# Optimization experiments

Measured on AMD Instinct MI355X. Metric: run time of the kernel, lower is better.

The kernel has to match this reference:

```python
import jax, jax.numpy as jnp
import numpy as np

B, H, L, D = 1, 8, 2048, 64
DP = 3   # positional coord dim
RE = 1   # extra relative features appended via concat
F = DP + RE  # LazyLinear in-features


def setup_inputs() -> dict:
    key = jax.random.key(0)
    ks = jax.random.split(key, 12)
    return {
        "q": jax.random.normal(ks[0], (B, H, L, D), jnp.float32),
        "k": jax.random.normal(ks[1], (B, H, L, D), jnp.float32),
        "v": jax.random.normal(ks[2], (B, H, L, D), jnp.float32),
        "c": jax.random.uniform(ks[3], (B, 1, 1, L), jnp.float32),
        "d_q": jax.random.normal(ks[4], (B, L, DP), jnp.float32),
        "d_k_top": jax.random.normal(ks[5], (B, L, DP), jnp.float32),
        "d_k_bot": jax.random.normal(ks[6], (B, L, DP), jnp.float32),
        "d_k_score": jax.random.uniform(ks[7], (B, L, 2, F), jnp.float32),
        "relative_top": jax.random.normal(ks[8], (B, L, L, RE), jnp.float32),
        "relative_bottom": jax.random.normal(ks[9], (B, L, L, RE), jnp.float32),
        "W_w": jax.random.normal(ks[10], (F, H), jnp.float32) * 0.1,
        "W_b": jax.random.normal(ks[11], (F, H), jnp.float32) * 0.1,
    }


def _pairwise_diff(a, b):
    # a: [B,Lq,Dp], b: [B,Lk,Dp] -> [B,Lq,Lk,Dp]
    return a[:, :, None, :] - b[:, None, :, :]


def reference(q, k, v, c, d_q, d_k_top, d_k_bot, d_k_score,
              relative_top, relative_bottom, W_w, W_b):
    # score function: scaled dot product -> [B,H,Lq,Lk]
    scores = jnp.einsum('bhqd,bhkd->bhqk', q, k) * (q.shape[-1] ** -0.5)

    # relative-position bias path
    dt = jnp.concatenate([_pairwise_diff(d_q, d_k_top), relative_top], axis=-1)     # [B,Lq,Lk,F]
    db = jnp.concatenate([_pairwise_diff(d_q, d_k_bot), relative_bottom], axis=-1)  # [B,Lq,Lk,F]
    dm = jnp.stack([dt, db], axis=3)                 # [B,Lq,Lk,2,F]
    dm = dm * d_k_score[:, None]                     # broadcast over Lq
    dm = dm.sum(axis=3)                              # [B,Lq,Lk,F]

    w = jax.nn.softplus(dm @ W_w).transpose(0, 3, 1, 2)  # [B,H,Lq,Lk]
    b = (dm @ W_b).transpose(0, 3, 1, 2)                 # [B,H,Lq,Lk]
    scores = scores * w + b

    # leaky probability function: softmax gated by per-key sampling weights c
    probs = jax.nn.softmax(scores, axis=-1) * c      # [B,H,Lq,Lk]

    out = jnp.einsum('bhqk,bhkd->bhqd', probs, v)
    return out, probs
```

## Files before the change

### kernel.cpp

```cpp
#include <hip/hip_runtime.h>
#include <cstdint>
#include <cstddef>

#define NH 8
#define LQ 2048
#define DH 64
#define NKT_HALF 16

typedef __attribute__((ext_vector_type(8))) __bf16 bf16x8;
typedef __attribute__((ext_vector_type(8))) unsigned short ushort8;
typedef __attribute__((ext_vector_type(4))) float floatx4;

__device__ __forceinline__ unsigned short bf_trunc(float x) {
    return (unsigned short)(__float_as_uint(x) >> 16);
}
__device__ __forceinline__ float bf_up(unsigned short h) {
    return __uint_as_float(((unsigned int)h) << 16);
}
__device__ __forceinline__ unsigned short bf_rne(float x) {
    unsigned int u = __float_as_uint(x);
    return (unsigned short)((u + 0x7FFFu + ((u >> 16) & 1u)) >> 16);
}
struct hl_t { unsigned short h, l; };
__device__ __forceinline__ hl_t split2(float x) {
    hl_t r;
    r.h = bf_trunc(x);
    r.l = bf_trunc(x - bf_up(r.h));
    return r;
}

#define MFMA16(A, B, C) __builtin_amdgcn_mfma_f32_16x16x32_bf16((A), (B), (C), 0, 0, 0)

__global__ __launch_bounds__(256) void prep_kernel(
    const float* __restrict__ kp,  const float* __restrict__ vp,
    const float* __restrict__ cp,  const float* __restrict__ dktp,
    const float* __restrict__ dkbp,const float* __restrict__ dksp,
    const float* __restrict__ Wwp, const float* __restrict__ Wbp,
    unsigned short* __restrict__ khig, unsigned short* __restrict__ klog,
    unsigned short* __restrict__ vhig, unsigned short* __restrict__ vlog,
    float* __restrict__ metag)
{
    const int bid = blockIdx.x;
    const int t   = threadIdx.x;

    if (bid < 256) {
        const int h = bid >> 5, kt = bid & 31;
        const int row = t >> 2, s = t & 3;
        const size_t kg = (size_t)(h * LQ) + kt * 64 + row;
        const float* src = kp + kg * DH + s * 16;
        unsigned short* dh_ = khig + kg * DH + s * 16;
        unsigned short* dl_ = klog + kg * DH + s * 16;
        ushort8 vh0, vh1, vl0, vl1;
#pragma unroll
        for (int j = 0; j < 2; ++j) {
            float4 x = *(const float4*)(src + 4 * j);
            hl_t a = split2(x.x * 0.125f), b = split2(x.y * 0.125f);
            hl_t c = split2(x.z * 0.125f), d = split2(x.w * 0.125f);
            vh0[4*j+0]=a.h; vl0[4*j+0]=a.l; vh0[4*j+1]=b.h; vl0[4*j+1]=b.l;
            vh0[4*j+2]=c.h; vl0[4*j+2]=c.l; vh0[4*j+3]=d.h; vl0[4*j+3]=d.l;
        }
#pragma unroll
        for (int j = 0; j < 2; ++j) {
            float4 x = *(const float4*)(src + 8 + 4 * j);
            hl_t a = split2(x.x * 0.125f), b = split2(x.y * 0.125f);
            hl_t c = split2(x.z * 0.125f), d = split2(x.w * 0.125f);
            vh1[4*j+0]=a.h; vl1[4*j+0]=a.l; vh1[4*j+1]=b.h; vl1[4*j+1]=b.l;
            vh1[4*j+2]=c.h; vl1[4*j+2]=c.l; vh1[4*j+3]=d.h; vl1[4*j+3]=d.l;
        }
        *(ushort8*)&dh_[0] = vh0; *(ushort8*)&dh_[8] = vh1;
        *(ushort8*)&dl_[0] = vl0; *(ushort8*)&dl_[8] = vl1;
    } else if (bid < 512) {
        const int h = (bid - 256) >> 5, kt = (bid - 256) & 31;
        const int p = t >> 4, mm = t & 15;
        const int k0 = kt * 64;
#pragma unroll
        for (int g = 0; g < 2; ++g) {
            const int kka = 2 * p + 32 * g;
            const float ca = cp[k0 + kka], cb = cp[k0 + kka + 1];
            const float* va = vp + ((size_t)(h * LQ + k0 + kka)) * DH;
            const float* vb = va + DH;
#pragma unroll
            for (int dd = 0; dd < 4; ++dd) {
                const int d = mm + 16 * dd;
                hl_t xa = split2(va[d] * ca);
                hl_t xb = split2(vb[d] * cb);
                const size_t base = ((size_t)(h * 32 + kt) * 64 + d) * 64 + kka;
                *(unsigned int*)&vhig[base] = (unsigned int)xa.h | ((unsigned int)xb.h << 16);
                *(unsigned int*)&vlog[base] = (unsigned int)xa.l | ((unsigned int)xb.l << 16);
            }
        }
    } else {
        const int idx = (bid - 512) * 256 + t;
        const int h  = idx >> 11;
        const int kg = idx & 2047;
        float Ww[4], Wb[4];
#pragma unroll
        for (int f = 0; f < 4; ++f) { Ww[f] = Wwp[f * NH + h]; Wb[f] = Wbp[f * NH + h]; }
        const float* sc_ = dksp + (size_t)kg * 8;
        const float* tp  = dktp + (size_t)kg * 3;
        const float* bt  = dkbp + (size_t)kg * 3;
        float* mo = metag + ((size_t)(h * LQ) + kg) * 12;
        float cw = 0.f, cb2 = 0.f;
#pragma unroll
        for (int f = 0; f < 3; ++f) {
            const float stf = sc_[f], sbf = sc_[4 + f];
            const float A  = stf + sbf;
            const float Bv = tp[f] * stf + bt[f] * sbf;
            mo[f]     = A * Ww[f];
            mo[4 + f] = A * Wb[f];
            cw  -= Bv * Ww[f];
            cb2 -= Bv * Wb[f];
        }
        mo[3]  = cw;              mo[7]  = cb2;
        mo[8]  = sc_[3] * Ww[3];  mo[9]  = sc_[7] * Ww[3];
        mo[10] = sc_[3] * Wb[3];  mo[11] = sc_[7] * Wb[3];
    }
}

template<int PRE>
__global__ __launch_bounds__(256, 3) void attn_main(
    const float* __restrict__ qp,  const float* __restrict__ kp,
    const float* __restrict__ vp,  const float* __restrict__ cp,
    const float* __restrict__ dqp, const float* __restrict__ dktp,
    const float* __restrict__ dkbp,const float* __restrict__ dksp,
    const float* __restrict__ rtp, const float* __restrict__ rbp,
    const float* __restrict__ Wwp, const float* __restrict__ Wbp,
    const unsigned short* __restrict__ khig, const unsigned short* __restrict__ klog,
    const unsigned short* __restrict__ vhig, const unsigned short* __restrict__ vlog,
    const float* __restrict__ metag,
    float* __restrict__ probp, float* __restrict__ lws, float* __restrict__ pvws)
{
    __shared__ unsigned short sh_khi[64 * 72];
    __shared__ unsigned short sh_klo[64 * 72];
    __shared__ unsigned short sh_vhi[64 * 72];
    __shared__ unsigned short sh_vlo[64 * 72];
    __shared__ float sh_meta[64 * 12];
    __shared__ float sh_dqs[64 * 3];

    const int bid  = blockIdx.x;
    const int half = bid & 1;
    const int h    = (bid >> 1) & 7;
    const int qt   = bid >> 4;
    const int q0   = qt * 64;
    const int t    = threadIdx.x;
    const int lane = t & 63;
    const int m    = lane & 15;
    const int quad = lane >> 4;
    const int w16  = (t >> 6) * 16;

    float Ww[4], Wb[4];
    if constexpr (!PRE) {
#pragma unroll
        for (int f = 0; f < 4; ++f) { Ww[f] = Wwp[f * NH + h]; Wb[f] = Wbp[f * NH + h]; }
    }

    {
        const int row = t >> 2, s = t & 3;
        const float* src = qp + ((size_t)(h * LQ + q0 + row)) * DH + s * 16;
        ushort8 vh0, vh1, vl0, vl1;
#pragma unroll
        for (int j = 0; j < 2; ++j) {
            float4 x = *(const float4*)(src + 4 * j);
            hl_t a = split2(x.x), b = split2(x.y), c = split2(x.z), d = split2(x.w);
            vh0[4*j+0]=a.h; vl0[4*j+0]=a.l; vh0[4*j+1]=b.h; vl0[4*j+1]=b.l;
            vh0[4*j+2]=c.h; vl0[4*j+2]=c.l; vh0[4*j+3]=d.h; vl0[4*j+3]=d.l;
        }
#pragma unroll
        for (int j = 0; j < 2; ++j) {
            float4 x = *(const float4*)(src + 8 + 4 * j);
            hl_t a = split2(x.x), b = split2(x.y), c = split2(x.z), d = split2(x.w);
            vh1[4*j+0]=a.h; vl1[4*j+0]=a.l; vh1[4*j+1]=b.h; vl1[4*j+1]=b.l;
            vh1[4*j+2]=c.h; vl1[4*j+2]=c.l; vh1[4*j+3]=d.h; vl1[4*j+3]=d.l;
        }
        const int base = row * 72 + s * 16;
        *(ushort8*)&sh_khi[base] = vh0;  *(ushort8*)&sh_khi[base + 8] = vh1;
        *(ushort8*)&sh_klo[base] = vl0;  *(ushort8*)&sh_klo[base + 8] = vl1;
        if (t < 64) {
            sh_dqs[t * 3 + 0] = dqp[(q0 + t) * 3 + 0];
            sh_dqs[t * 3 + 1] = dqp[(q0 + t) * 3 + 1];
            sh_dqs[t * 3 + 2] = dqp[(q0 + t) * 3 + 2];
        }
    }
    __syncthreads();

    bf16x8 aqh[2], aql[2];
#pragma unroll
    for (int kc = 0; kc < 2; ++kc) {
        aqh[kc] = *(const bf16x8*)&sh_khi[(w16 + m) * 72 + kc * 32 + quad * 8];
        aql[kc] = *(const bf16x8*)&sh_klo[(w16 + m) * 72 + kc * 32 + quad * 8];
    }
    float dq0[4], dq1[4], dq2[4];
#pragma unroll
    for (int r = 0; r < 4; ++r) {
        const int row = w16 + quad * 4 + r;
        dq0[r] = sh_dqs[row * 3 + 0]; dq1[r] = sh_dqs[row * 3 + 1]; dq2[r] = sh_dqs[row * 3 + 2];
    }
    __syncthreads();

    const floatx4 zf = {0.f, 0.f, 0.f, 0.f};
    floatx4 pacc[4] = {zf, zf, zf, zf};
    float lpart[4] = {0.f, 0.f, 0.f, 0.f};

    for (int kth = 0; kth < NKT_HALF; ++kth) {
        const int k0 = (half * NKT_HALF + kth) * 64;

        if constexpr (PRE) {
            {
                const int row = t >> 2, s = t & 3;
                const size_t gb = ((size_t)(h * LQ) + k0 + row) * DH + s * 16;
                const int base = row * 72 + s * 16;
                *(ushort8*)&sh_khi[base]     = *(const ushort8*)&khig[gb];
                *(ushort8*)&sh_khi[base + 8] = *(const ushort8*)&khig[gb + 8];
                *(ushort8*)&sh_klo[base]     = *(const ushort8*)&klog[gb];
                *(ushort8*)&sh_klo[base + 8] = *(const ushort8*)&klog[gb + 8];
            }
            {
                const int row = t >> 2, s = t & 3;
                const size_t gb = ((size_t)(h * 32 + (k0 >> 6)) * 64 + row) * 64 + s * 16;
                const int base = row * 72 + s * 16;
                *(ushort8*)&sh_vhi[base]     = *(const ushort8*)&vhig[gb];
                *(ushort8*)&sh_vhi[base + 8] = *(const ushort8*)&vhig[gb + 8];
                *(ushort8*)&sh_vlo[base]     = *(const ushort8*)&vlog[gb];
                *(ushort8*)&sh_vlo[base + 8] = *(const ushort8*)&vlog[gb + 8];
            }
            if (t < 192) {
                const int k = t / 3, j = t - k * 3;
                const float4 mv = *(const float4*)(metag + ((size_t)(h * LQ) + k0 + k) * 12 + j * 4);
                *(float4*)&sh_meta[k * 12 + j * 4] = mv;
            }
        } else {
            {
                const int row = t >> 2, s = t & 3;
                const float* src = kp + ((size_t)(h * LQ + k0 + row)) * DH + s * 16;
                ushort8 vh0, vh1, vl0, vl1;
#pragma unroll
                for (int j = 0; j < 2; ++j) {
                    float4 x = *(const float4*)(src + 4 * j);
                    hl_t a = split2(x.x), b = split2(x.y), c = split2(x.z), d = split2(x.w);
                    vh0[4*j+0]=a.h; vl0[4*j+0]=a.l; vh0[4*j+1]=b.h; vl0[4*j+1]=b.l;
                    vh0[4*j+2]=c.h; vl0[4*j+2]=c.l; vh0[4*j+3]=d.h; vl0[4*j+3]=d.l;
                }
#pragma unroll
                for (int j = 0; j < 2; ++j) {
                    float4 x = *(const float4*)(src + 8 + 4 * j);
                    hl_t a = split2(x.x), b = split2(x.y), c = split2(x.z), d = split2(x.w);
                    vh1[4*j+0]=a.h; vl1[4*j+0]=a.l; vh1[4*j+1]=b.h; vl1[4*j+1]=b.l;
                    vh1[4*j+2]=c.h; vl1[4*j+2]=c.l; vh1[4*j+3]=d.h; vl1[4*j+3]=d.l;
                }
                const int base = row * 72 + s * 16;
                *(ushort8*)&sh_khi[base] = vh0;  *(ushort8*)&sh_khi[base + 8] = vh1;
                *(ushort8*)&sh_klo[base] = vl0;  *(ushort8*)&sh_klo[base + 8] = vl1;
            }
            {
                const int p = t >> 4;
                const int mm = t & 15;
#pragma unroll
                for (int g = 0; g < 2; ++g) {
                    const int kka = 2 * p + 32 * g;
                    const float ca = cp[k0 + kka], cb = cp[k0 + kka + 1];
                    const float* va = vp + ((size_t)(h * LQ + k0 + kka)) * DH;
                    const float* vb = va + DH;
#pragma unroll
                    for (int dd = 0; dd < 4; ++dd) {
                        const int d = mm + 16 * dd;
                        hl_t xa = split2(va[d] * ca);
                        hl_t xb = split2(vb[d] * cb);
                        *(unsigned int*)&sh_vhi[d * 72 + kka] = (unsigned int)xa.h | ((unsigned int)xb.h << 16);
                        *(unsigned int*)&sh_vlo[d * 72 + kka] = (unsigned int)xa.l | ((unsigned int)xb.l << 16);
                    }
                }
            }
            if (t < 64) {
                const int kg = k0 + t;
                const float* sc_ = dksp + (size_t)kg * 8;
                const float* tp  = dktp + (size_t)kg * 3;
                const float* bt  = dkbp + (size_t)kg * 3;
                float cw = 0.f, cb2 = 0.f;
#pragma unroll
                for (int f = 0; f < 3; ++f) {
                    const float stf = sc_[f], sbf = sc_[4 + f];
                    const float A  = stf + sbf;
                    const float Bv = tp[f] * stf + bt[f] * sbf;
                    sh_meta[t * 12 + f]     = A * Ww[f];
                    sh_meta[t * 12 + 4 + f] = A * Wb[f];
                    cw  -= Bv * Ww[f];
                    cb2 -= Bv * Wb[f];
                }
                sh_meta[t * 12 + 3]  = cw;              sh_meta[t * 12 + 7]  = cb2;
                sh_meta[t * 12 + 8]  = sc_[3] * Ww[3];  sh_meta[t * 12 + 9]  = sc_[7] * Ww[3];
                sh_meta[t * 12 + 10] = sc_[3] * Wb[3];  sh_meta[t * 12 + 11] = sc_[7] * Wb[3];
            }
        }
        __syncthreads();

        float rt_[4][4], rb_[4][4];
#pragma unroll
        for (int r = 0; r < 4; ++r) {
            const size_t q = (size_t)(q0 + w16 + quad * 4 + r);
#pragma unroll
            for (int nt = 0; nt < 4; ++nt) {
                rt_[nt][r] = rtp[q * LQ + k0 + nt * 16 + m];
                rb_[nt][r] = rbp[q * LQ + k0 + nt * 16 + m];
            }
        }

        floatx4 sc[4] = {zf, zf, zf, zf};
#pragma unroll
        for (int nt = 0; nt < 4; ++nt) {
#pragma unroll
            for (int kc = 0; kc < 2; ++kc) {
                const int kb = (nt * 16 + m) * 72 + kc * 32 + quad * 8;
                bf16x8 bh = *(const bf16x8*)&sh_khi[kb];
                bf16x8 bl = *(const bf16x8*)&sh_klo[kb];
                sc[nt] = MFMA16(aqh[kc], bh, sc[nt]);
                sc[nt] = MFMA16(aql[kc], bh, sc[nt]);
                sc[nt] = MFMA16(aqh[kc], bl, sc[nt]);
            }
        }
        __syncthreads();

        unsigned short* ebf = sh_klo;
#pragma unroll
        for (int nt = 0; nt < 4; ++nt) {
            const int kcol = nt * 16 + m;
            const float m0 = sh_meta[kcol * 12 + 0],  m1 = sh_meta[kcol * 12 + 1];
            const float m2 = sh_meta[kcol * 12 + 2],  m3 = sh_meta[kcol * 12 + 3];
            const float m4 = sh_meta[kcol * 12 + 4],  m5 = sh_meta[kcol * 12 + 5];
            const float m6 = sh_meta[kcol * 12 + 6],  m7 = sh_meta[kcol * 12 + 7];
            const float m8 = sh_meta[kcol * 12 + 8],  m9 = sh_meta[kcol * 12 + 9];
            const float mA = sh_meta[kcol * 12 + 10], mB = sh_meta[kcol * 12 + 11];
#pragma unroll
            for (int r = 0; r < 4; ++r) {
                float ww = fmaf(dq0[r], m0, m3); ww = fmaf(dq1[r], m1, ww); ww = fmaf(dq2[r], m2, ww);
                ww = fmaf(rt_[nt][r], m8, ww);   ww = fmaf(rb_[nt][r], m9, ww);
                float bb = fmaf(dq0[r], m4, m7); bb = fmaf(dq1[r], m5, bb); bb = fmaf(dq2[r], m6, bb);
                bb = fmaf(rt_[nt][r], mA, bb);   bb = fmaf(rb_[nt][r], mB, bb);
                const float wg = fmaxf(ww, 0.f) + __logf(1.f + __expf(-fabsf(ww)));
                float sv;
                if constexpr (PRE) sv = fmaf(sc[nt][r], wg, bb);
                else               sv = fmaf(sc[nt][r] * 0.125f, wg, bb);
                const float e  = __expf(sv - 8.0f);
                lpart[r] += e;
                probp[((size_t)(h * LQ + q0 + w16 + quad * 4 + r)) * LQ + k0 + kcol] = e;
                ebf[(w16 + quad * 4 + r) * 72 + kcol] = bf_rne(e);
            }
        }

        bf16x8 ap0 = *(const bf16x8*)&ebf[(w16 + m) * 72 + quad * 8];
        bf16x8 ap1 = *(const bf16x8*)&ebf[(w16 + m) * 72 + 32 + quad * 8];
#pragma unroll
        for (int nt = 0; nt < 4; ++nt) {
            const int vb = (nt * 16 + m) * 72 + quad * 8;
            bf16x8 bh0 = *(const bf16x8*)&sh_vhi[vb];
            bf16x8 bl0 = *(const bf16x8*)&sh_vlo[vb];
            bf16x8 bh1 = *(const bf16x8*)&sh_vhi[vb + 32];
            bf16x8 bl1 = *(const bf16x8*)&sh_vlo[vb + 32];
            pacc[nt] = MFMA16(ap0, bh0, pacc[nt]);
            pacc[nt] = MFMA16(ap0, bl0, pacc[nt]);
            pacc[nt] = MFMA16(ap1, bh1, pacc[nt]);
            pacc[nt] = MFMA16(ap1, bl1, pacc[nt]);
        }
        __syncthreads();
    }

#pragma unroll
    for (int off = 1; off < 16; off <<= 1) {
#pragma unroll
        for (int r = 0; r < 4; ++r) lpart[r] += __shfl_xor(lpart[r], off, 64);
    }
    if (m == 0) {
#pragma unroll
        for (int r = 0; r < 4; ++r)
            lws[half * (NH * LQ) + h * LQ + q0 + w16 + quad * 4 + r] = lpart[r];
    }
#pragma unroll
    for (int nt = 0; nt < 4; ++nt) {
#pragma unroll
        for (int r = 0; r < 4; ++r) {
            const size_t row = (size_t)(h * LQ + q0 + w16 + quad * 4 + r);
            pvws[(size_t)half * (NH * LQ * DH) + row * DH + nt * 16 + m] = pacc[nt][r];
        }
    }
}

__global__ void combine_kernel(const float* __restrict__ pvws, const float* __restrict__ lws,
                               float* __restrict__ outp)
{
    const int idx4 = blockIdx.x * 256 + threadIdx.x;
    const int row  = idx4 >> 4;
    const int d4   = (idx4 & 15) * 4;
    const float4 a = *(const float4*)(pvws + (size_t)row * DH + d4);
    const float4 b = *(const float4*)(pvws + (size_t)(NH * LQ * DH) + (size_t)row * DH + d4);
    const float rl = 1.0f / (lws[row] + lws[NH * LQ + row]);
    *(float4*)(outp + (size_t)row * DH + d4) =
        make_float4((a.x + b.x) * rl, (a.y + b.y) * rl, (a.z + b.z) * rl, (a.w + b.w) * rl);
}

__global__ void norm_kernel(float* __restrict__ probp, const float* __restrict__ cp,
                            const float* __restrict__ lws)
{
    const int row = blockIdx.x;
    const float rl = 1.0f / (lws[row] + lws[NH * LQ + row]);
    float* p = probp + (size_t)row * LQ;
    const int t = threadIdx.x;
    float4 x0 = *(const float4*)(p + t * 4);
    float4 x1 = *(const float4*)(p + (t + 256) * 4);
    const float4 c0 = *(const float4*)(cp + t * 4);
    const float4 c1 = *(const float4*)(cp + (t + 256) * 4);
    x0.x *= rl * c0.x; x0.y *= rl * c0.y; x0.z *= rl * c0.z; x0.w *= rl * c0.w;
    x1.x *= rl * c1.x; x1.y *= rl * c1.y; x1.z *= rl * c1.z; x1.w *= rl * c1.w;
    *(float4*)(p + t * 4)         = x0;
    *(float4*)(p + (t + 256) * 4) = x1;
}

extern "C" void kernel_launch(void* const* d_in, const int* in_sizes, int n_in,
                              void* d_out, int out_size, void* d_ws, size_t ws_size,
                              hipStream_t stream)
{
    (void)in_sizes; (void)n_in; (void)out_size;
    const float* qp   = (const float*)d_in[0];
    const float* kp   = (const float*)d_in[1];
    const float* vp   = (const float*)d_in[2];
    const float* cp   = (const float*)d_in[3];
    const float* dqp  = (const float*)d_in[4];
    const float* dktp = (const float*)d_in[5];
    const float* dkbp = (const float*)d_in[6];
    const float* dksp = (const float*)d_in[7];
    const float* rtp  = (const float*)d_in[8];
    const float* rbp  = (const float*)d_in[9];
    const float* Wwp  = (const float*)d_in[10];
    const float* Wbp  = (const float*)d_in[11];

    float* outp  = (float*)d_out;
    float* probp = (float*)d_out + (size_t)NH * LQ * DH;

    float* lws  = (float*)d_ws;
    float* pvws = lws + 2 * (NH * LQ);
    unsigned short* khig = (unsigned short*)(pvws + (size_t)2 * NH * LQ * DH);
    unsigned short* klog = khig + (size_t)NH * LQ * DH;
    unsigned short* vhig = klog + (size_t)NH * LQ * DH;
    unsigned short* vlog = vhig + (size_t)NH * LQ * DH;
    float* metag = (float*)(vlog + (size_t)NH * LQ * DH);

    const size_t need = (size_t)2 * NH * LQ * 4
                      + (size_t)2 * NH * LQ * DH * 4
                      + (size_t)4 * NH * LQ * DH * 2
                      + (size_t)NH * LQ * 12 * 4;

    if (ws_size >= need) {
        prep_kernel<<<dim3(576), dim3(256), 0, stream>>>(
            kp, vp, cp, dktp, dkbp, dksp, Wwp, Wbp, khig, klog, vhig, vlog, metag);
        attn_main<1><<<dim3(512), dim3(256), 0, stream>>>(
            qp, kp, vp, cp, dqp, dktp, dkbp, dksp, rtp, rbp, Wwp, Wbp,
            khig, klog, vhig, vlog, metag, probp, lws, pvws);
    } else {
        attn_main<0><<<dim3(512), dim3(256), 0, stream>>>(
            qp, kp, vp, cp, dqp, dktp, dkbp, dksp, rtp, rbp, Wwp, Wbp,
            nullptr, nullptr, nullptr, nullptr, nullptr, probp, lws, pvws);
    }
    combine_kernel<<<dim3(1024), dim3(256), 0, stream>>>(pvws, lws, outp);
    norm_kernel<<<dim3(NH * LQ), dim3(256), 0, stream>>>(probp, cp, lws);
}
```

Measured before the change: 287.3 us.

## Prefetch next K/V/meta tile into registers and fuse norm with combine

Removes the non-precomputed fallback path, so the precomputed split-bf16 K/V tiles are always used. The main loop now loads the next tile's K/V/meta into registers while the current tile is being computed, which hides global load latency behind the math. Launch bounds drop from 3 to 2 waves per SIMD to make room for the extra registers. The separate combine and norm kernels become one kernel that handles 8 rows per block, cutting a launch and reusing the c vector across rows. The trade-off is lower occupancy, and the workspace size check is dropped.

Result: no change. 286.2 us (-0.4%).

```diff
diff --git a/kernel.cpp b/kernel.cpp
--- a/kernel.cpp
+++ b/kernel.cpp
@@ -117,14 +117,9 @@
     }
 }
 
-template<int PRE>
-__global__ __launch_bounds__(256, 3) void attn_main(
-    const float* __restrict__ qp,  const float* __restrict__ kp,
-    const float* __restrict__ vp,  const float* __restrict__ cp,
-    const float* __restrict__ dqp, const float* __restrict__ dktp,
-    const float* __restrict__ dkbp,const float* __restrict__ dksp,
+__global__ __launch_bounds__(256, 2) void attn_main(
+    const float* __restrict__ qp,  const float* __restrict__ dqp,
     const float* __restrict__ rtp, const float* __restrict__ rbp,
-    const float* __restrict__ Wwp, const float* __restrict__ Wbp,
     const unsigned short* __restrict__ khig, const unsigned short* __restrict__ klog,
     const unsigned short* __restrict__ vhig, const unsigned short* __restrict__ vlog,
     const float* __restrict__ metag,
@@ -148,15 +143,27 @@
     const int quad = lane >> 4;
     const int w16  = (t >> 6) * 16;
 
-    float Ww[4], Wb[4];
-    if constexpr (!PRE) {
-#pragma unroll
-        for (int f = 0; f < 4; ++f) { Ww[f] = Wwp[f * NH + h]; Wb[f] = Wbp[f * NH + h]; }
-    }
+    const int srow = t >> 2, ss = t & 3;
+    const int sbase = srow * 72 + ss * 16;
+    const int mk = t / 3, mj = t - mk * 3;
+
+    size_t kgb = ((size_t)(h * LQ) + half * NKT_HALF * 64 + srow) * DH + ss * 16;
+    size_t vgb = ((size_t)(h * 32 + half * NKT_HALF) * 64 + srow) * 64 + ss * 16;
+    size_t mgb = ((size_t)(h * LQ) + half * NKT_HALF * 64 + mk) * 12 + mj * 4;
+
+    ushort8 rkh0 = *(const ushort8*)&khig[kgb];
+    ushort8 rkh1 = *(const ushort8*)&khig[kgb + 8];
+    ushort8 rkl0 = *(const ushort8*)&klog[kgb];
+    ushort8 rkl1 = *(const ushort8*)&klog[kgb + 8];
+    ushort8 rvh0 = *(const ushort8*)&vhig[vgb];
+    ushort8 rvh1 = *(const ushort8*)&vhig[vgb + 8];
+    ushort8 rvl0 = *(const ushort8*)&vlog[vgb];
+    ushort8 rvl1 = *(const ushort8*)&vlog[vgb + 8];
+    float4  rmeta;
+    if (t < 192) rmeta = *(const float4*)&metag[mgb];
 
     {
-        const int row = t >> 2, s = t & 3;
-        const float* src = qp + ((size_t)(h * LQ + q0 + row)) * DH + s * 16;
+        const float* src = qp + ((size_t)(h * LQ + q0 + srow)) * DH + ss * 16;
         ushort8 vh0, vh1, vl0, vl1;
 #pragma unroll
         for (int j = 0; j < 2; ++j) {
@@ -172,9 +179,8 @@
             vh1[4*j+0]=a.h; vl1[4*j+0]=a.l; vh1[4*j+1]=b.h; vl1[4*j+1]=b.l;
             vh1[4*j+2]=c.h; vl1[4*j+2]=c.l; vh1[4*j+3]=d.h; vl1[4*j+3]=d.l;
         }
-        const int base = row * 72 + s * 16;
-        *(ushort8*)&sh_khi[base] = vh0;  *(ushort8*)&sh_khi[base + 8] = vh1;
-        *(ushort8*)&sh_klo[base] = vl0;  *(ushort8*)&sh_klo[base + 8] = vl1;
+        *(ushort8*)&sh_khi[sbase] = vh0;  *(ushort8*)&sh_khi[sbase + 8] = vh1;
+        *(ushort8*)&sh_klo[sbase] = vl0;  *(ushort8*)&sh_klo[sbase + 8] = vl1;
         if (t < 64) {
             sh_dqs[t * 3 + 0] = dqp[(q0 + t) * 3 + 0];
             sh_dqs[t * 3 + 1] = dqp[(q0 + t) * 3 + 1];
@@ -204,94 +210,31 @@
     for (int kth = 0; kth < NKT_HALF; ++kth) {
         const int k0 = (half * NKT_HALF + kth) * 64;
 
-        if constexpr (PRE) {
-            {
-                const int row = t >> 2, s = t & 3;
-                const size_t gb = ((size_t)(h * LQ) + k0 + row) * DH + s * 16;
-                const int base = row * 72 + s * 16;
-                *(ushort8*)&sh_khi[base]     = *(const ushort8*)&khig[gb];
-                *(ushort8*)&sh_khi[base + 8] = *(const ushort8*)&khig[gb + 8];
-                *(ushort8*)&sh_klo[base]     = *(const ushort8*)&klog[gb];
-                *(ushort8*)&sh_klo[base + 8] = *(const ushort8*)&klog[gb + 8];
-            }
-            {
-                const int row = t >> 2, s = t & 3;
-                const size_t gb = ((size_t)(h * 32 + (k0 >> 6)) * 64 + row) * 64 + s * 16;
-                const int base = row * 72 + s * 16;
-                *(ushort8*)&sh_vhi[base]     = *(const ushort8*)&vhig[gb];
-                *(ushort8*)&sh_vhi[base + 8] = *(const ushort8*)&vhig[gb + 8];
-                *(ushort8*)&sh_vlo[base]     = *(const ushort8*)&vlog[gb];
-                *(ushort8*)&sh_vlo[base + 8] = *(const ushort8*)&vlog[gb + 8];
-            }
-            if (t < 192) {
-                const int k = t / 3, j = t - k * 3;
-                const float4 mv = *(const float4*)(metag + ((size_t)(h * LQ) + k0 + k) * 12 + j * 4);
-                *(float4*)&sh_meta[k * 12 + j * 4] = mv;
-            }
-        } else {
-            {
-                const int row = t >> 2, s = t & 3;
-                const float* src = kp + ((size_t)(h * LQ + k0 + row)) * DH + s * 16;
-                ushort8 vh0, vh1, vl0, vl1;
-#pragma unroll
-                for (int j = 0; j < 2; ++j) {
-                    float4 x = *(const float4*)(src + 4 * j);
-                    hl_t a = split2(x.x), b = split2(x.y), c = split2(x.z), d = split2(x.w);
-                    vh0[4*j+0]=a.h; vl0[4*j+0]=a.l; vh0[4*j+1]=b.h; vl0[4*j+1]=b.l;
-                    vh0[4*j+2]=c.h; vl0[4*j+2]=c.l; vh0[4*j+3]=d.h; vl0[4*j+3]=d.l;
-                }
-#pragma unroll
-                for (int j = 0; j < 2; ++j) {
-                    float4 x = *(const float4*)(src + 8 + 4 * j);
-                    hl_t a = split2(x.x), b = split2(x.y), c = split2(x.z), d = split2(x.w);
-                    vh1[4*j+0]=a.h; vl1[4*j+0]=a.l; vh1[4*j+1]=b.h; vl1[4*j+1]=b.l;
-                    vh1[4*j+2]=c.h; vl1[4*j+2]=c.l; vh1[4*j+3]=d.h; vl1[4*j+3]=d.l;
-                }
-                const int base = row * 72 + s * 16;
-                *(ushort8*)&sh_khi[base] = vh0;  *(ushort8*)&sh_khi[base + 8] = vh1;
-                *(ushort8*)&sh_klo[base] = vl0;  *(ushort8*)&sh_klo[base + 8] = vl1;
-            }
-            {
-                const int p = t >> 4;
-                const int mm = t & 15;
-#pragma unroll
-                for (int g = 0; g < 2; ++g) {
-                    const int kka = 2 * p + 32 * g;
-                    const float ca = cp[k0 + kka], cb = cp[k0 + kka + 1];
-                    const float* va = vp + ((size_t)(h * LQ + k0 + kka)) * DH;
-                    const float* vb = va + DH;
-#pragma unroll
-                    for (int dd = 0; dd < 4; ++dd) {
-                        const int d = mm + 16 * dd;
-                        hl_t xa = split2(va[d] * ca);
-                        hl_t xb = split2(vb[d] * cb);
-                        *(unsigned int*)&sh_vhi[d * 72 + kka] = (unsigned int)xa.h | ((unsigned int)xb.h << 16);
-                        *(unsigned int*)&sh_vlo[d * 72 + kka] = (unsigned int)xa.l | ((unsigned int)xb.l << 16);
-                    }
-                }
-            }
-            if (t < 64) {
-                const int kg = k0 + t;
-                const float* sc_ = dksp + (size_t)kg * 8;
-                const float* tp  = dktp + (size_t)kg * 3;
-                const float* bt  = dkbp + (size_t)kg * 3;
-                float cw = 0.f, cb2 = 0.f;
-#pragma unroll
-                for (int f = 0; f < 3; ++f) {
-                    const float stf = sc_[f], sbf = sc_[4 + f];
-                    const float A  = stf + sbf;
-                    const float Bv = tp[f] * stf + bt[f] * sbf;
-                    sh_meta[t * 12 + f]     = A * Ww[f];
-                    sh_meta[t * 12 + 4 + f] = A * Wb[f];
-                    cw  -= Bv * Ww[f];
-                    cb2 -= Bv * Wb[f];
-                }
-                sh_meta[t * 12 + 3]  = cw;              sh_meta[t * 12 + 7]  = cb2;
-                sh_meta[t * 12 + 8]  = sc_[3] * Ww[3];  sh_meta[t * 12 + 9]  = sc_[7] * Ww[3];
-                sh_meta[t * 12 + 10] = sc_[3] * Wb[3];  sh_meta[t * 12 + 11] = sc_[7] * Wb[3];
-            }
-        }
+        *(ushort8*)&sh_khi[sbase]     = rkh0;
+        *(ushort8*)&sh_khi[sbase + 8] = rkh1;
+        *(ushort8*)&sh_klo[sbase]     = rkl0;
+        *(ushort8*)&sh_klo[sbase + 8] = rkl1;
+        *(ushort8*)&sh_vhi[sbase]     = rvh0;
+        *(ushort8*)&sh_vhi[sbase + 8] = rvh1;
+        *(ushort8*)&sh_vlo[sbase]     = rvl0;
+        *(ushort8*)&sh_vlo[sbase + 8] = rvl1;
+        if (t < 192) *(float4*)&sh_meta[mk * 12 + mj * 4] = rmeta;
         __syncthreads();
+
+        if (kth + 1 < NKT_HALF) {
+            kgb += (size_t)64 * DH;
+            vgb += (size_t)64 * 64;
+            mgb += (size_t)64 * 12;
+            rkh0 = *(const ushort8*)&khig[kgb];
+            rkh1 = *(const ushort8*)&khig[kgb + 8];
+            rkl0 = *(const ushort8*)&klog[kgb];
+            rkl1 = *(const ushort8*)&klog[kgb + 8];
+            rvh0 = *(const ushort8*)&vhig[vgb];
+            rvh1 = *(const ushort8*)&vhig[vgb + 8];
+            rvl0 = *(const ushort8*)&vlog[vgb];
+            rvl1 = *(const ushort8*)&vlog[vgb + 8];
+            if (t < 192) rmeta = *(const float4*)&metag[mgb];
+        }
 
         float rt_[4][4], rb_[4][4];
 #pragma unroll
@@ -336,9 +279,7 @@
                 float bb = fmaf(dq0[r], m4, m7); bb = fmaf(dq1[r], m5, bb); bb = fmaf(dq2[r], m6, bb);
                 bb = fmaf(rt_[nt][r], mA, bb);   bb = fmaf(rb_[nt][r], mB, bb);
                 const float wg = fmaxf(ww, 0.f) + __logf(1.f + __expf(-fabsf(ww)));
-                float sv;
-                if constexpr (PRE) sv = fmaf(sc[nt][r], wg, bb);
-                else               sv = fmaf(sc[nt][r] * 0.125f, wg, bb);
+                const float sv = fmaf(sc[nt][r], wg, bb);
                 const float e  = __expf(sv - 8.0f);
                 lpart[r] += e;
                 probp[((size_t)(h * LQ + q0 + w16 + quad * 4 + r)) * LQ + k0 + kcol] = e;
@@ -383,41 +324,43 @@
     }
 }
 
-__global__ void combine_kernel(const float* __restrict__ pvws, const float* __restrict__ lws,
-                               float* __restrict__ outp)
+__global__ __launch_bounds__(256) void norm_combine(
+    float* __restrict__ probp, const float* __restrict__ cp,
+    const float* __restrict__ lws, const float* __restrict__ pvws,
+    float* __restrict__ outp)
 {
-    const int idx4 = blockIdx.x * 256 + threadIdx.x;
-    const int row  = idx4 >> 4;
-    const int d4   = (idx4 & 15) * 4;
-    const float4 a = *(const float4*)(pvws + (size_t)row * DH + d4);
-    const float4 b = *(const float4*)(pvws + (size_t)(NH * LQ * DH) + (size_t)row * DH + d4);
-    const float rl = 1.0f / (lws[row] + lws[NH * LQ + row]);
-    *(float4*)(outp + (size_t)row * DH + d4) =
-        make_float4((a.x + b.x) * rl, (a.y + b.y) * rl, (a.z + b.z) * rl, (a.w + b.w) * rl);
-}
-
-__global__ void norm_kernel(float* __restrict__ probp, const float* __restrict__ cp,
-                            const float* __restrict__ lws)
-{
-    const int row = blockIdx.x;
-    const float rl = 1.0f / (lws[row] + lws[NH * LQ + row]);
-    float* p = probp + (size_t)row * LQ;
-    const int t = threadIdx.x;
-    float4 x0 = *(const float4*)(p + t * 4);
-    float4 x1 = *(const float4*)(p + (t + 256) * 4);
+    __shared__ float rl8[8];
+    const int t    = threadIdx.x;
+    const int row0 = blockIdx.x * 8;
     const float4 c0 = *(const float4*)(cp + t * 4);
     const float4 c1 = *(const float4*)(cp + (t + 256) * 4);
-    x0.x *= rl * c0.x; x0.y *= rl * c0.y; x0.z *= rl * c0.z; x0.w *= rl * c0.w;
-    x1.x *= rl * c1.x; x1.y *= rl * c1.y; x1.z *= rl * c1.z; x1.w *= rl * c1.w;
-    *(float4*)(p + t * 4)         = x0;
-    *(float4*)(p + (t + 256) * 4) = x1;
+    if (t < 8) rl8[t] = 1.0f / (lws[row0 + t] + lws[NH * LQ + row0 + t]);
+    __syncthreads();
+#pragma unroll 2
+    for (int rr = 0; rr < 8; ++rr) {
+        const float rl = rl8[rr];
+        float* p = probp + (size_t)(row0 + rr) * LQ;
+        float4 x0 = *(const float4*)(p + t * 4);
+        float4 x1 = *(const float4*)(p + (t + 256) * 4);
+        x0.x *= rl * c0.x; x0.y *= rl * c0.y; x0.z *= rl * c0.z; x0.w *= rl * c0.w;
+        x1.x *= rl * c1.x; x1.y *= rl * c1.y; x1.z *= rl * c1.z; x1.w *= rl * c1.w;
+        *(float4*)(p + t * 4)         = x0;
+        *(float4*)(p + (t + 256) * 4) = x1;
+    }
+#pragma unroll
+    for (int j = 0; j < 2; ++j) {
+        const int lin = j * 256 + t;
+        const int rr  = lin >> 6, d = lin & 63;
+        const size_t rowd = (size_t)(row0 + rr) * DH + d;
+        outp[rowd] = (pvws[rowd] + pvws[(size_t)(NH * LQ * DH) + rowd]) * rl8[rr];
+    }
 }
 
 extern "C" void kernel_launch(void* const* d_in, const int* in_sizes, int n_in,
                               void* d_out, int out_size, void* d_ws, size_t ws_size,
                               hipStream_t stream)
 {
-    (void)in_sizes; (void)n_in; (void)out_size;
+    (void)in_sizes; (void)n_in; (void)out_size; (void)ws_size;
     const float* qp   = (const float*)d_in[0];
     const float* kp   = (const float*)d_in[1];
     const float* vp   = (const float*)d_in[2];
@@ -442,22 +385,9 @@
     unsigned short* vlog = vhig + (size_t)NH * LQ * DH;
     float* metag = (float*)(vlog + (size_t)NH * LQ * DH);
 
-    const size_t need = (size_t)2 * NH * LQ * 4
-                      + (size_t)2 * NH * LQ * DH * 4
-                      + (size_t)4 * NH * LQ * DH * 2
-                      + (size_t)NH * LQ * 12 * 4;
-
-    if (ws_size >= need) {
-        prep_kernel<<<dim3(576), dim3(256), 0, stream>>>(
-            kp, vp, cp, dktp, dkbp, dksp, Wwp, Wbp, khig, klog, vhig, vlog, metag);
-        attn_main<1><<<dim3(512), dim3(256), 0, stream>>>(
-            qp, kp, vp, cp, dqp, dktp, dkbp, dksp, rtp, rbp, Wwp, Wbp,
-            khig, klog, vhig, vlog, metag, probp, lws, pvws);
-    } else {
-        attn_main<0><<<dim3(512), dim3(256), 0, stream>>>(
-            qp, kp, vp, cp, dqp, dktp, dkbp, dksp, rtp, rbp, Wwp, Wbp,
-            nullptr, nullptr, nullptr, nullptr, nullptr, probp, lws, pvws);
-    }
-    combine_kernel<<<dim3(1024), dim3(256), 0, stream>>>(pvws, lws, outp);
-    norm_kernel<<<dim3(NH * LQ), dim3(256), 0, stream>>>(probp, cp, lws);
-}
+    prep_kernel<<<dim3(576), dim3(256), 0, stream>>>(
+        kp, vp, cp, dktp, dkbp, dksp, Wwp, Wbp, khig, klog, vhig, vlog, metag);
+    attn_main<<<dim3(512), dim3(256), 0, stream>>>(
+        qp, dqp, rtp, rbp, khig, klog, vhig, vlog, metag, probp, lws, pvws);
+    norm_combine<<<dim3(2048), dim3(256), 0, stream>>>(probp, cp, lws, pvws, outp);
+}
```
